# Kernel tuning notes

Measured on AMD Instinct MI355X. Metric: run time of the kernel, lower is better.

Reference implementation:

```python
import jax, jax.numpy as jnp
import numpy as np

ACTION_WEIGHT = 10.0
ACTION_DIM = 4
OBS_DIM = 128


def setup_inputs() -> dict:
    key = jax.random.key(0)
    k1, k2 = jax.random.split(key)
    B, H, T = 64, 32, ACTION_DIM + 256 * OBS_DIM  # 32772
    preds = jax.random.normal(k1, (B, H, T), dtype=jnp.float32)
    targ = jax.random.normal(k2, (B, H, T), dtype=jnp.float32)
    return {"preds": preds, "targ": targ}


def _chamfer(x, y):
    # x: [G, Nx, D] (gts), y: [G, Ny, D] (preds)
    # P[g, i, j] = ||x_i||^2 + ||y_j||^2 - 2 x_i . y_j
    x2 = jnp.sum(x * x, axis=-1)          # [G, Nx]
    y2 = jnp.sum(y * y, axis=-1)          # [G, Ny]
    zz = jnp.einsum('gnd,gmd->gnm', x, y)  # [G, Nx, Ny]
    P = x2[:, :, None] + y2[:, None, :] - 2.0 * zz
    loss_1 = jnp.sum(jnp.min(P, axis=1), axis=1)  # min over x points, sum over y points
    loss_2 = jnp.sum(jnp.min(P, axis=2), axis=1)  # min over y points, sum over x points
    return loss_1 + loss_2  # [G]


def reference(preds, targ):
    B, H, T = preds.shape
    actions = preds[:, :, :ACTION_DIM]
    action_targs = targ[:, :, :ACTION_DIM]
    action_loss = jnp.mean((actions - action_targs) ** 2, axis=-1)  # [B, H]
    a0_loss = jnp.mean(action_loss[:, 0])
    action_loss = action_loss.at[:, 0].multiply(ACTION_WEIGHT)
    action_loss = jnp.mean(action_loss)

    obs = preds[:, :, ACTION_DIM:].reshape(B, H, -1, OBS_DIM)
    obs_targ = targ[:, :, ACTION_DIM:].reshape(B, H, -1, OBS_DIM)
    N = obs.shape[2]
    # Vectorize the per-horizon loop: fold (B, H) into one batched dim.
    x = obs_targ.reshape(B * H, N, OBS_DIM)
    y = obs.reshape(B * H, N, OBS_DIM)
    ch = _chamfer(x, y)  # [B*H]
    # sum_h mean_b(ch[:, h]) / H == mean over (B*H)
    chamfer_loss = jnp.mean(ch)

    return (action_loss + chamfer_loss, a0_loss)
```

## Files before the change

kernel.cpp:

```cpp
#include <hip/hip_runtime.h>
#include <hip/hip_bf16.h>

#define T_DIM 32772
#define NGROUP 2048

typedef short short8v __attribute__((ext_vector_type(8)));
typedef float float4v __attribute__((ext_vector_type(4)));
typedef unsigned int uint4v __attribute__((ext_vector_type(4)));

__device__ __forceinline__ unsigned int f2bf2(float a, float b) {
    __hip_bfloat162 h = __float22bfloat162_rn(make_float2(a, b));
    union { __hip_bfloat162 h; unsigned int u; } c; c.h = h;
    return c.u;
}

__device__ __forceinline__ short8v pack8(const float4v u0, const float4v u1) {
    uint4v p;
    p[0] = f2bf2(u0[0], u0[1]);
    p[1] = f2bf2(u0[2], u0[3]);
    p[2] = f2bf2(u1[0], u1[1]);
    p[3] = f2bf2(u1[2], u1[3]);
    return __builtin_bit_cast(short8v, p);
}

__global__ __launch_bounds__(512) void chamfer_kernel(
    const float* __restrict__ preds, const float* __restrict__ targ,
    float* __restrict__ ch_out)
{
    __shared__ __align__(16) unsigned short Ys[256 * 128];
    __shared__ float y2s[256];
    __shared__ float x2s[256];
    __shared__ float redA[8];
    __shared__ float redB[4];
    float* colmin_alias = reinterpret_cast<float*>(&Ys[0]);

    const int g = blockIdx.x;
    const float* gx = targ  + (size_t)g * T_DIM + 4;
    const float* gy = preds + (size_t)g * T_DIM + 4;

    const int tid  = threadIdx.x;
    const int lane = tid & 63;
    const int w    = tid >> 6;
    const int lg   = lane >> 4;
    const int lc   = lane & 15;

    char* Ysb = (char*)Ys;

    short8v a_frag[2][4];
    #pragma unroll
    for (int ti = 0; ti < 2; ++ti) {
        const float* xr = gx + (size_t)(w * 32 + ti * 16 + lc) * 128;
        float ss = 0.f;
        #pragma unroll
        for (int kk = 0; kk < 4; ++kk) {
            const float4v u0 = *reinterpret_cast<const float4v*>(xr + kk * 32 + lg * 8);
            const float4v u1 = *reinterpret_cast<const float4v*>(xr + kk * 32 + lg * 8 + 4);
            ss += u0[0]*u0[0] + u0[1]*u0[1] + u0[2]*u0[2] + u0[3]*u0[3];
            ss += u1[0]*u1[0] + u1[1]*u1[1] + u1[2]*u1[2] + u1[3]*u1[3];
            a_frag[ti][kk] = pack8(u0, u1);
        }
        ss += __shfl_xor(ss, 16);
        ss += __shfl_xor(ss, 32);
        if (lg == 0) x2s[w * 32 + ti * 16 + lc] = ss;
    }

    {
        const int prow = tid >> 1;
        const int h2   = tid & 1;
        const float* src = gy + (size_t)prow * 128 + h2 * 64;
        float ss = 0.f;
        #pragma unroll
        for (int j = 0; j < 4; ++j) {
            const float4v u0 = *reinterpret_cast<const float4v*>(src + j * 16);
            const float4v u1 = *reinterpret_cast<const float4v*>(src + j * 16 + 4);
            const float4v u2 = *reinterpret_cast<const float4v*>(src + j * 16 + 8);
            const float4v u3 = *reinterpret_cast<const float4v*>(src + j * 16 + 12);
            ss += u0[0]*u0[0] + u0[1]*u0[1] + u0[2]*u0[2] + u0[3]*u0[3];
            ss += u1[0]*u1[0] + u1[1]*u1[1] + u1[2]*u1[2] + u1[3]*u1[3];
            ss += u2[0]*u2[0] + u2[1]*u2[1] + u2[2]*u2[2] + u2[3]*u2[3];
            ss += u3[0]*u3[0] + u3[1]*u3[1] + u3[2]*u3[2] + u3[3]*u3[3];
            const int c0 = h2 * 8 + 2 * j;
            const int c1 = c0 + 1;
            const int o0 = prow * 256 + ((((c0 & 7) + prow) & 7) << 4) + ((c0 & 8) << 4);
            const int o1 = prow * 256 + ((((c1 & 7) + prow) & 7) << 4) + ((c1 & 8) << 4);
            *reinterpret_cast<short8v*>(Ysb + o0) = pack8(u0, u1);
            *reinterpret_cast<short8v*>(Ysb + o1) = pack8(u2, u3);
        }
        ss += __shfl_xor(ss, 1);
        if (h2 == 0) y2s[prow] = ss;
    }
    __syncthreads();

    float rowmin[2][4];
    #pragma unroll
    for (int ti = 0; ti < 2; ++ti)
        #pragma unroll
        for (int r = 0; r < 4; ++r) rowmin[ti][r] = 1e30f;
    float cmin[4];

    const int rs0 = ((lg + lc) & 7) << 4;
    const int rs1 = ((lg + lc + 4) & 7) << 4;
    const int x2byte = (w * 32 + lg * 4) * 4;

    #pragma unroll
    for (int tj = 0; tj < 16; ++tj) {
        const int rbyte = (tj * 16 + lc) * 256;
        const float y2c = y2s[tj * 16 + lc];

        float4v acc0 = {0.f, 0.f, 0.f, 0.f};
        float4v acc1 = {0.f, 0.f, 0.f, 0.f};
        {
            short8v b0 = *reinterpret_cast<const short8v*>(Ysb + rbyte + rs0);
            short8v b1 = *reinterpret_cast<const short8v*>(Ysb + rbyte + rs1);
            acc0 = __builtin_amdgcn_mfma_f32_16x16x32_bf16(a_frag[0][0], b0, acc0, 0, 0, 0);
            acc1 = __builtin_amdgcn_mfma_f32_16x16x32_bf16(a_frag[1][0], b0, acc1, 0, 0, 0);
            acc0 = __builtin_amdgcn_mfma_f32_16x16x32_bf16(a_frag[0][1], b1, acc0, 0, 0, 0);
            acc1 = __builtin_amdgcn_mfma_f32_16x16x32_bf16(a_frag[1][1], b1, acc1, 0, 0, 0);
            b0 = *reinterpret_cast<const short8v*>(Ysb + rbyte + 128 + rs0);
            b1 = *reinterpret_cast<const short8v*>(Ysb + rbyte + 128 + rs1);
            acc0 = __builtin_amdgcn_mfma_f32_16x16x32_bf16(a_frag[0][2], b0, acc0, 0, 0, 0);
            acc1 = __builtin_amdgcn_mfma_f32_16x16x32_bf16(a_frag[1][2], b0, acc1, 0, 0, 0);
            acc0 = __builtin_amdgcn_mfma_f32_16x16x32_bf16(a_frag[0][3], b1, acc0, 0, 0, 0);
            acc1 = __builtin_amdgcn_mfma_f32_16x16x32_bf16(a_frag[1][3], b1, acc1, 0, 0, 0);
        }

        float cminv = 1e30f;
        {
            const float4v x2a = *reinterpret_cast<const float4v*>((const char*)x2s + x2byte);
            #pragma unroll
            for (int r = 0; r < 4; ++r) {
                const float t = -2.0f * acc0[r];
                rowmin[0][r] = fminf(rowmin[0][r], y2c + t);
                cminv = fminf(cminv, x2a[r] + t);
            }
        }
        {
            const float4v x2b = *reinterpret_cast<const float4v*>((const char*)x2s + x2byte + 64);
            #pragma unroll
            for (int r = 0; r < 4; ++r) {
                const float t = -2.0f * acc1[r];
                rowmin[1][r] = fminf(rowmin[1][r], y2c + t);
                cminv = fminf(cminv, x2b[r] + t);
            }
        }
        cminv = fminf(cminv, __shfl_xor(cminv, 16));
        cminv = fminf(cminv, __shfl_xor(cminv, 32));
        if (lg == (tj & 3)) cmin[tj >> 2] = cminv + y2c;
    }

    __syncthreads();

    #pragma unroll
    for (int s = 0; s < 4; ++s)
        colmin_alias[w * 256 + s * 64 + lane] = cmin[s];

    float s2 = 0.f;
    #pragma unroll
    for (int ti = 0; ti < 2; ++ti) {
        const float4v x2v = *reinterpret_cast<const float4v*>((const char*)x2s + x2byte + ti * 64);
        #pragma unroll
        for (int r = 0; r < 4; ++r) {
            float v = rowmin[ti][r];
            v = fminf(v, __shfl_xor(v, 1));
            v = fminf(v, __shfl_xor(v, 2));
            v = fminf(v, __shfl_xor(v, 4));
            v = fminf(v, __shfl_xor(v, 8));
            s2 += x2v[r] + v;
        }
    }
    s2 += __shfl_xor(s2, 16);
    s2 += __shfl_xor(s2, 32);
    if (lane == 0) redA[w] = s2;
    __syncthreads();

    if (tid < 256) {
        float m = colmin_alias[tid];
        #pragma unroll
        for (int ww = 1; ww < 8; ++ww) m = fminf(m, colmin_alias[ww * 256 + tid]);
        #pragma unroll
        for (int s = 1; s < 64; s <<= 1) m += __shfl_xor(m, s);
        if (lane == 0) redB[w] = m;
    }
    __syncthreads();
    if (tid == 0) {
        const float l1 = redB[0] + redB[1] + redB[2] + redB[3];
        float l2 = 0.f;
        #pragma unroll
        for (int ww = 0; ww < 8; ++ww) l2 += redA[ww];
        ch_out[g] = l1 + l2;
    }
}

__global__ __launch_bounds__(256) void final_kernel(
    const float* __restrict__ preds, const float* __restrict__ targ,
    const float* __restrict__ ch, float* __restrict__ out)
{
    __shared__ float rsw[4], rsa[4], rsc[4];
    const int tid = threadIdx.x;
    const int lane = tid & 63, w = tid >> 6;
    float sw = 0.f, sa0 = 0.f, sc = 0.f;
    for (int p = tid; p < NGROUP; p += 256) {
        const float* pp = preds + (size_t)p * T_DIM;
        const float* tt = targ  + (size_t)p * T_DIM;
        float al = 0.f;
        #pragma unroll
        for (int d = 0; d < 4; ++d) { const float df = pp[d] - tt[d]; al += df * df; }
        al *= 0.25f;
        if ((p & 31) == 0) { sw += 10.f * al; sa0 += al; }
        else               { sw += al; }
        sc += ch[p];
    }
    #pragma unroll
    for (int s = 1; s < 64; s <<= 1) {
        sw  += __shfl_xor(sw, s);
        sa0 += __shfl_xor(sa0, s);
        sc  += __shfl_xor(sc, s);
    }
    if (lane == 0) { rsw[w] = sw; rsa[w] = sa0; rsc[w] = sc; }
    __syncthreads();
    if (tid == 0) {
        float tsw = 0.f, tsa = 0.f, tsc = 0.f;
        #pragma unroll
        for (int i = 0; i < 4; ++i) { tsw += rsw[i]; tsa += rsa[i]; tsc += rsc[i]; }
        out[0] = tsw / 2048.f + tsc / 2048.f;
        out[1] = tsa / 64.f;
    }
}

extern "C" void kernel_launch(void* const* d_in, const int* in_sizes, int n_in,
                              void* d_out, int out_size, void* d_ws, size_t ws_size,
                              hipStream_t stream) {
    const float* preds = (const float*)d_in[0];
    const float* targ  = (const float*)d_in[1];
    float* out = (float*)d_out;
    float* ch  = (float*)d_ws;
    chamfer_kernel<<<NGROUP, 512, 0, stream>>>(preds, targ, ch);
    final_kernel<<<1, 256, 0, stream>>>(preds, targ, ch, out);
}
```

Baseline: 128.5 us.

## Stream preds tiles via global_load_lds DMA with double-buffered bf16 conversion

Instead of loading all 256 pred rows up front and converting them before any MFMA work, the kernel now streams the preds in eight 32-row fp32 chunks. Each chunk goes global->LDS through global_load_lds, then is converted to a double-buffered bf16 tile while the next chunk's DMA is in flight. This aims to overlap global memory latency with MFMA compute. In exchange it adds a barrier per chunk and an fp32 staging buffer. The single shared Fs staging buffer is overwritten by the next DMA only after the conversion reads, which relies on the waitcnt and barrier ordering.

```diff
diff --git a/kernel.cpp b/kernel.cpp
--- a/kernel.cpp
+++ b/kernel.cpp
@@ -7,6 +7,7 @@
 typedef short short8v __attribute__((ext_vector_type(8)));
 typedef float float4v __attribute__((ext_vector_type(4)));
 typedef unsigned int uint4v __attribute__((ext_vector_type(4)));
+typedef unsigned int uint2v __attribute__((ext_vector_type(2)));
 
 __device__ __forceinline__ unsigned int f2bf2(float a, float b) {
     __hip_bfloat162 h = __float22bfloat162_rn(make_float2(a, b));
@@ -23,16 +24,23 @@
     return __builtin_bit_cast(short8v, p);
 }
 
+__device__ __forceinline__ void dma16(const void* g, void* l) {
+    __builtin_amdgcn_global_load_lds(
+        (const __attribute__((address_space(1))) unsigned int*)g,
+        (__attribute__((address_space(3))) unsigned int*)l, 16, 0, 0);
+}
+
 __global__ __launch_bounds__(512) void chamfer_kernel(
     const float* __restrict__ preds, const float* __restrict__ targ,
     float* __restrict__ ch_out)
 {
-    __shared__ __align__(16) unsigned short Ys[256 * 128];
+    __shared__ __align__(16) float Fs[4096];
+    __shared__ __align__(16) unsigned short Bs[2][4096];
     __shared__ float y2s[256];
     __shared__ float x2s[256];
     __shared__ float redA[8];
     __shared__ float redB[4];
-    float* colmin_alias = reinterpret_cast<float*>(&Ys[0]);
+    float* colmin_alias = &Fs[0];
 
     const int g = blockIdx.x;
     const float* gx = targ  + (size_t)g * T_DIM + 4;
@@ -44,7 +52,51 @@
     const int lg   = lane >> 4;
     const int lc   = lane & 15;
 
-    char* Ysb = (char*)Ys;
+    char* Fsb = (char*)Fs;
+    char* Bsb = (char*)Bs;
+
+    auto dma_chunk = [&](int c) {
+        const char* src = (const char*)gy + (size_t)c * 16384;
+        const int o0 = w * 1024;
+        const int o1 = w * 1024 + 8192;
+        dma16(src + o0 + lane * 16, Fsb + o0);
+        dma16(src + o1 + lane * 16, Fsb + o1);
+    };
+
+    auto cvt_chunk = [&](int c, int bufsel) {
+        const float4v u0 = *reinterpret_cast<const float4v*>(Fsb + tid * 16);
+        const float4v u1 = *reinterpret_cast<const float4v*>(Fsb + 8192 + tid * 16);
+        float s0 = u0[0]*u0[0] + u0[1]*u0[1] + u0[2]*u0[2] + u0[3]*u0[3];
+        float s1 = u1[0]*u1[0] + u1[1]*u1[1] + u1[2]*u1[2] + u1[3]*u1[3];
+        #pragma unroll
+        for (int s = 1; s < 32; s <<= 1) {
+            s0 += __shfl_xor(s0, s);
+            s1 += __shfl_xor(s1, s);
+        }
+        const int r1 = tid >> 5;
+        if ((lane & 31) == 0) {
+            y2s[c * 32 + r1]      = s0;
+            y2s[c * 32 + 16 + r1] = s1;
+        }
+        const int col4 = tid & 31;
+        const int c16  = col4 >> 1;
+        const int sub  = (col4 & 1) * 8;
+        char* B = Bsb + bufsel * 8192;
+        {
+            uint2v p; p[0] = f2bf2(u0[0], u0[1]); p[1] = f2bf2(u0[2], u0[3]);
+            const int o = r1 * 256 + ((((c16 & 7) + r1) & 7) << 4) + ((c16 & 8) << 4) + sub;
+            *reinterpret_cast<uint2v*>(B + o) = p;
+        }
+        {
+            const int r2 = 16 + r1;
+            uint2v p; p[0] = f2bf2(u1[0], u1[1]); p[1] = f2bf2(u1[2], u1[3]);
+            const int o = r2 * 256 + ((((c16 & 7) + r2) & 7) << 4) + ((c16 & 8) << 4) + sub;
+            *reinterpret_cast<uint2v*>(B + o) = p;
+        }
+    };
+
+    dma_chunk(0);
+    __builtin_amdgcn_sched_barrier(0);
 
     short8v a_frag[2][4];
     #pragma unroll
@@ -64,33 +116,6 @@
         if (lg == 0) x2s[w * 32 + ti * 16 + lc] = ss;
     }
 
-    {
-        const int prow = tid >> 1;
-        const int h2   = tid & 1;
-        const float* src = gy + (size_t)prow * 128 + h2 * 64;
-        float ss = 0.f;
-        #pragma unroll
-        for (int j = 0; j < 4; ++j) {
-            const float4v u0 = *reinterpret_cast<const float4v*>(src + j * 16);
-            const float4v u1 = *reinterpret_cast<const float4v*>(src + j * 16 + 4);
-            const float4v u2 = *reinterpret_cast<const float4v*>(src + j * 16 + 8);
-            const float4v u3 = *reinterpret_cast<const float4v*>(src + j * 16 + 12);
-            ss += u0[0]*u0[0] + u0[1]*u0[1] + u0[2]*u0[2] + u0[3]*u0[3];
-            ss += u1[0]*u1[0] + u1[1]*u1[1] + u1[2]*u1[2] + u1[3]*u1[3];
-            ss += u2[0]*u2[0] + u2[1]*u2[1] + u2[2]*u2[2] + u2[3]*u2[3];
-            ss += u3[0]*u3[0] + u3[1]*u3[1] + u3[2]*u3[2] + u3[3]*u3[3];
-            const int c0 = h2 * 8 + 2 * j;
-            const int c1 = c0 + 1;
-            const int o0 = prow * 256 + ((((c0 & 7) + prow) & 7) << 4) + ((c0 & 8) << 4);
-            const int o1 = prow * 256 + ((((c1 & 7) + prow) & 7) << 4) + ((c1 & 8) << 4);
-            *reinterpret_cast<short8v*>(Ysb + o0) = pack8(u0, u1);
-            *reinterpret_cast<short8v*>(Ysb + o1) = pack8(u2, u3);
-        }
-        ss += __shfl_xor(ss, 1);
-        if (h2 == 0) y2s[prow] = ss;
-    }
-    __syncthreads();
-
     float rowmin[2][4];
     #pragma unroll
     for (int ti = 0; ti < 2; ++ti)
@@ -102,53 +127,74 @@
     const int rs1 = ((lg + lc + 4) & 7) << 4;
     const int x2byte = (w * 32 + lg * 4) * 4;
 
-    #pragma unroll
-    for (int tj = 0; tj < 16; ++tj) {
-        const int rbyte = (tj * 16 + lc) * 256;
-        const float y2c = y2s[tj * 16 + lc];
-
-        float4v acc0 = {0.f, 0.f, 0.f, 0.f};
-        float4v acc1 = {0.f, 0.f, 0.f, 0.f};
-        {
-            short8v b0 = *reinterpret_cast<const short8v*>(Ysb + rbyte + rs0);
-            short8v b1 = *reinterpret_cast<const short8v*>(Ysb + rbyte + rs1);
-            acc0 = __builtin_amdgcn_mfma_f32_16x16x32_bf16(a_frag[0][0], b0, acc0, 0, 0, 0);
-            acc1 = __builtin_amdgcn_mfma_f32_16x16x32_bf16(a_frag[1][0], b0, acc1, 0, 0, 0);
-            acc0 = __builtin_amdgcn_mfma_f32_16x16x32_bf16(a_frag[0][1], b1, acc0, 0, 0, 0);
-            acc1 = __builtin_amdgcn_mfma_f32_16x16x32_bf16(a_frag[1][1], b1, acc1, 0, 0, 0);
-            b0 = *reinterpret_cast<const short8v*>(Ysb + rbyte + 128 + rs0);
-            b1 = *reinterpret_cast<const short8v*>(Ysb + rbyte + 128 + rs1);
-            acc0 = __builtin_amdgcn_mfma_f32_16x16x32_bf16(a_frag[0][2], b0, acc0, 0, 0, 0);
-            acc1 = __builtin_amdgcn_mfma_f32_16x16x32_bf16(a_frag[1][2], b0, acc1, 0, 0, 0);
-            acc0 = __builtin_amdgcn_mfma_f32_16x16x32_bf16(a_frag[0][3], b1, acc0, 0, 0, 0);
-            acc1 = __builtin_amdgcn_mfma_f32_16x16x32_bf16(a_frag[1][3], b1, acc1, 0, 0, 0);
-        }
-
-        float cminv = 1e30f;
-        {
-            const float4v x2a = *reinterpret_cast<const float4v*>((const char*)x2s + x2byte);
-            #pragma unroll
-            for (int r = 0; r < 4; ++r) {
-                const float t = -2.0f * acc0[r];
-                rowmin[0][r] = fminf(rowmin[0][r], y2c + t);
-                cminv = fminf(cminv, x2a[r] + t);
+    asm volatile("s_waitcnt vmcnt(0)" ::: "memory");
+    __builtin_amdgcn_sched_barrier(0);
+    cvt_chunk(0, 0);
+    dma_chunk(1);
+    asm volatile("s_waitcnt lgkmcnt(0)" ::: "memory");
+    __builtin_amdgcn_s_barrier();
+    __builtin_amdgcn_sched_barrier(0);
+
+    #pragma unroll
+    for (int c = 0; c < 8; ++c) {
+        const char* B = Bsb + (c & 1) * 8192;
+        #pragma unroll
+        for (int tjl = 0; tjl < 2; ++tjl) {
+            const int tj = c * 2 + tjl;
+            const int rbyte = (tjl * 16 + lc) * 256;
+            const float y2c = y2s[c * 32 + tjl * 16 + lc];
+
+            float4v acc0 = {0.f, 0.f, 0.f, 0.f};
+            float4v acc1 = {0.f, 0.f, 0.f, 0.f};
+            {
+                short8v b0 = *reinterpret_cast<const short8v*>(B + rbyte + rs0);
+                short8v b1 = *reinterpret_cast<const short8v*>(B + rbyte + rs1);
+                acc0 = __builtin_amdgcn_mfma_f32_16x16x32_bf16(a_frag[0][0], b0, acc0, 0, 0, 0);
+                acc1 = __builtin_amdgcn_mfma_f32_16x16x32_bf16(a_frag[1][0], b0, acc1, 0, 0, 0);
+                acc0 = __builtin_amdgcn_mfma_f32_16x16x32_bf16(a_frag[0][1], b1, acc0, 0, 0, 0);
+                acc1 = __builtin_amdgcn_mfma_f32_16x16x32_bf16(a_frag[1][1], b1, acc1, 0, 0, 0);
+                b0 = *reinterpret_cast<const short8v*>(B + rbyte + 128 + rs0);
+                b1 = *reinterpret_cast<const short8v*>(B + rbyte + 128 + rs1);
+                acc0 = __builtin_amdgcn_mfma_f32_16x16x32_bf16(a_frag[0][2], b0, acc0, 0, 0, 0);
+                acc1 = __builtin_amdgcn_mfma_f32_16x16x32_bf16(a_frag[1][2], b0, acc1, 0, 0, 0);
+                acc0 = __builtin_amdgcn_mfma_f32_16x16x32_bf16(a_frag[0][3], b1, acc0, 0, 0, 0);
+                acc1 = __builtin_amdgcn_mfma_f32_16x16x32_bf16(a_frag[1][3], b1, acc1, 0, 0, 0);
             }
-        }
-        {
-            const float4v x2b = *reinterpret_cast<const float4v*>((const char*)x2s + x2byte + 64);
-            #pragma unroll
-            for (int r = 0; r < 4; ++r) {
-                const float t = -2.0f * acc1[r];
-                rowmin[1][r] = fminf(rowmin[1][r], y2c + t);
-                cminv = fminf(cminv, x2b[r] + t);
+
+            float cminv = 1e30f;
+            {
+                const float4v x2a = *reinterpret_cast<const float4v*>((const char*)x2s + x2byte);
+                #pragma unroll
+                for (int r = 0; r < 4; ++r) {
+                    const float t = -2.0f * acc0[r];
+                    rowmin[0][r] = fminf(rowmin[0][r], y2c + t);
+                    cminv = fminf(cminv, x2a[r] + t);
+                }
             }
-        }
-        cminv = fminf(cminv, __shfl_xor(cminv, 16));
-        cminv = fminf(cminv, __shfl_xor(cminv, 32));
-        if (lg == (tj & 3)) cmin[tj >> 2] = cminv + y2c;
-    }
-
-    __syncthreads();
+            {
+                const float4v x2b = *reinterpret_cast<const float4v*>((const char*)x2s + x2byte + 64);
+                #pragma unroll
+                for (int r = 0; r < 4; ++r) {
+                    const float t = -2.0f * acc1[r];
+                    rowmin[1][r] = fminf(rowmin[1][r], y2c + t);
+                    cminv = fminf(cminv, x2b[r] + t);
+                }
+            }
+            cminv = fminf(cminv, __shfl_xor(cminv, 16));
+            cminv = fminf(cminv, __shfl_xor(cminv, 32));
+            if (lg == (tj & 3)) cmin[tj >> 2] = cminv + y2c;
+        }
+
+        if (c < 7) {
+            asm volatile("s_waitcnt vmcnt(0)" ::: "memory");
+            __builtin_amdgcn_sched_barrier(0);
+            cvt_chunk(c + 1, (c + 1) & 1);
+            if (c < 6) dma_chunk(c + 2);
+        }
+        asm volatile("s_waitcnt lgkmcnt(0)" ::: "memory");
+        __builtin_amdgcn_s_barrier();
+        __builtin_amdgcn_sched_barrier(0);
+    }
 
     #pragma unroll
     for (int s = 0; s < 4; ++s)
```

After: 143.0 us. 1.11x slower.
